# Kernel tuning notes

Measured on AMD Instinct MI355X. Metric: run time of the kernel, lower is better.

## Reference

```python
import jax, jax.numpy as jnp
import numpy as np

B, S, H, HKV, D = 1, 1024, 32, 8, 128
HID = H * D
GROUPS = H // HKV
ALPHA_K, ALPHA_V = 0.5, 0.5
GAMMA_MIN, GAMMA_MAX = 0.5, 2.0
ETA_MIN, ETA_MAX = 0.5, 2.0
BETA_BIAS, BIAS_CAP = 1.0, 5.0
BETA_POST = 0.5
ROPE_THETA = 10000.0


def setup_inputs() -> dict:
    key = jax.random.key(0)
    ks = jax.random.split(key, 9)
    hidden_states = jax.random.normal(ks[0], (B, S, HID), jnp.float32) * 0.02
    # additive causal mask (LLaMA-style, large negative above diagonal)
    causal = jnp.tril(jnp.ones((S, S), dtype=bool))
    attention_mask = jnp.where(causal, 0.0, -1e9).astype(jnp.float32)[None, None]
    position_ids = jnp.arange(S, dtype=jnp.int32)[None]
    sq = 1.0 / np.sqrt(HID)
    Wq = jax.random.normal(ks[1], (HID, HID), jnp.float32) * sq
    Wk = jax.random.normal(ks[2], (HKV * D, HID), jnp.float32) * sq
    Wv = jax.random.normal(ks[3], (HKV * D, HID), jnp.float32) * sq
    Wo = jax.random.normal(ks[4], (HID, HID), jnp.float32) * sq
    prior = jax.random.uniform(ks[5], (S,), jnp.float32)  # per-key-position prior, in [0,1)
    head_mask_l1 = (jax.random.uniform(ks[6], (H,)) > 0.5).astype(jnp.float32)
    head_mask_l2 = (jax.random.uniform(ks[7], (H,)) > 0.5).astype(jnp.float32)
    return {"hidden_states": hidden_states, "attention_mask": attention_mask,
            "position_ids": position_ids, "Wq": Wq, "Wk": Wk, "Wv": Wv, "Wo": Wo,
            "prior": prior, "head_mask_l1": head_mask_l1, "head_mask_l2": head_mask_l2}


def _rope(position_ids):
    inv_freq = 1.0 / (ROPE_THETA ** (jnp.arange(0, D, 2, dtype=jnp.float32) / D))
    freqs = position_ids.astype(jnp.float32)[..., None] * inv_freq  # [B,S,D/2]
    emb = jnp.concatenate([freqs, freqs], axis=-1)                  # [B,S,D]
    return jnp.cos(emb)[:, None], jnp.sin(emb)[:, None]             # [B,1,S,D]


def _rotate_half(x):
    x1, x2 = x[..., : D // 2], x[..., D // 2:]
    return jnp.concatenate([-x2, x1], axis=-1)


def reference(hidden_states, attention_mask, position_ids, Wq, Wk, Wv, Wo,
              prior, head_mask_l1, head_mask_l2):
    b, s, _ = hidden_states.shape
    # projections (Linear without bias: x @ W.T)
    q = (hidden_states @ Wq.T).reshape(b, s, H, D).transpose(0, 2, 1, 3)     # [B,H,S,D]
    k = (hidden_states @ Wk.T).reshape(b, s, HKV, D).transpose(0, 2, 1, 3)   # [B,Hkv,S,D]
    v = (hidden_states @ Wv.T).reshape(b, s, HKV, D).transpose(0, 2, 1, 3)
    cos, sin = _rope(position_ids)
    q = q * cos + _rotate_half(q) * sin
    k = k * cos + _rotate_half(k) * sin
    # repeat_kv: expand KV heads to match query heads (GQA)
    k = jnp.repeat(k, GROUPS, axis=1)  # [B,H,S,D]
    v = jnp.repeat(v, GROUPS, axis=1)
    # level4_scale: per-key-position multiplicative scaling of K and V
    gamma = jnp.clip(1.0 + ALPHA_K * prior, GAMMA_MIN, GAMMA_MAX)  # [S]
    eta = jnp.clip(1.0 + ALPHA_V * prior, ETA_MIN, ETA_MAX)
    k = k * gamma[None, None, :, None]
    v = v * eta[None, None, :, None]
    # attention logits
    attn = jnp.einsum('bhqd,bhkd->bhqk', q, k) / np.sqrt(D)
    # level1_bias: capped additive bias on logits, blended per-head
    bias = jnp.clip(BETA_BIAS * prior, -BIAS_CAP, BIAS_CAP)        # [S] over key dim
    steered = attn + bias[None, None, None, :]
    attn = attn + (steered - attn) * head_mask_l1[None, :, None, None]
    # causal mask
    attn = attn + attention_mask
    probs = jax.nn.softmax(attn.astype(jnp.float32), axis=-1)
    # level2_post: post-softmax rescale + renormalize, blended per-head
    sp = probs * (1.0 + BETA_POST * prior)[None, None, None, :]
    sp = sp / jnp.sum(sp, axis=-1, keepdims=True)
    probs = probs + (sp - probs) * head_mask_l2[None, :, None, None]
    out = jnp.einsum('bhqk,bhkd->bhqd', probs, v)                  # [B,H,S,D]
    out = out.transpose(0, 2, 1, 3).reshape(b, s, HID)
    return out @ Wo.T
```

## Files before the change

### kernel.cpp

```cpp
#include <hip/hip_runtime.h>
#include <math.h>

#define S_LEN 1024
#define HID_DIM 4096
#define NH 32
#define NKV 8
#define DH 128

typedef __attribute__((ext_vector_type(8))) short sh8;
typedef __attribute__((ext_vector_type(4))) short sh4;
typedef __attribute__((ext_vector_type(4))) float f4;

__device__ __forceinline__ unsigned short f2bf(float x) {
    union { float f; unsigned int u; } v; v.f = x;
    unsigned int r = v.u + 0x7FFFu + ((v.u >> 16) & 1u);
    return (unsigned short)(r >> 16);
}

__device__ __forceinline__ void gl_lds16(const unsigned short* g, unsigned short* l) {
    __builtin_amdgcn_global_load_lds(
        (const __attribute__((address_space(1))) unsigned int*)g,
        (__attribute__((address_space(3))) unsigned int*)l, 16, 0, 0);
}


__global__ void cvt_hw(const float* __restrict__ hidden, const float* __restrict__ Wq,
                       const float* __restrict__ Wk, const float* __restrict__ Wv,
                       unsigned short* __restrict__ hbf, unsigned short* __restrict__ wbuf)
{
    const int idx = blockIdx.x * 256 + threadIdx.x;
    const int NH4 = (S_LEN * HID_DIM) / 4;
    float4 v;
    sh4* dst;
    if (idx < NH4) {
        v = ((const float4*)hidden)[idx];
        dst = (sh4*)hbf + idx;
    } else {
        const int j = idx - NH4;
        const int row = j >> 10;
        if (row < 4096)      v = ((const float4*)Wq)[j];
        else if (row < 5120) v = ((const float4*)Wk)[j - 4096 * 1024];
        else                 v = ((const float4*)Wv)[j - 5120 * 1024];
        dst = (sh4*)wbuf + j;
    }
    sh4 o;
    o.x = (short)f2bf(v.x); o.y = (short)f2bf(v.y);
    o.z = (short)f2bf(v.z); o.w = (short)f2bf(v.w);
    *dst = o;
}

__global__ void cvt_wo(const float* __restrict__ Wo, unsigned short* __restrict__ wbuf)
{
    const int idx = blockIdx.x * 256 + threadIdx.x;
    const float4 v = ((const float4*)Wo)[idx];
    sh4 o;
    o.x = (short)f2bf(v.x); o.y = (short)f2bf(v.y);
    o.z = (short)f2bf(v.z); o.w = (short)f2bf(v.w);
    ((sh4*)wbuf)[idx] = o;
}

__global__ __launch_bounds__(256)
void gemm_bf16(const unsigned short* __restrict__ A, const unsigned short* __restrict__ B,
               float* __restrict__ C, int K, int kslices, int ldc)
{
    __shared__ __attribute__((aligned(16))) unsigned short sA[128 * 32];
    __shared__ __attribute__((aligned(16))) unsigned short sB[128 * 32];

    const int tid  = threadIdx.x;
    const int wave = tid >> 6;
    const int lane = tid & 63;
    const int l15  = lane & 15;
    const int quad = lane >> 4;
    const int m0   = blockIdx.y * 128;
    const int n0   = blockIdx.x * 128;
    const int wm   = (wave >> 1) * 64;
    const int wn   = (wave & 1) * 64;

    const int kchunk = K / kslices;
    const int kbeg = blockIdx.z * kchunk;
    const int kend = kbeg + kchunk;

    const int srow = wave * 32 + (lane >> 2);
    const int scol = (lane & 3) * 8;
    const unsigned short* Ag = A + (size_t)(m0 + srow) * K + scol;
    const unsigned short* Bg = B + (size_t)(n0 + srow) * K + scol;
    unsigned short* sAw = &sA[wave * 32 * 32];
    unsigned short* sBw = &sB[wave * 32 * 32];

    f4 acc[4][4];
#pragma unroll
    for (int i = 0; i < 4; i++)
#pragma unroll
        for (int j = 0; j < 4; j++)
            acc[i][j] = f4{0.0f, 0.0f, 0.0f, 0.0f};

    for (int k0 = kbeg; k0 < kend; k0 += 32) {
        __syncthreads();
        gl_lds16(Ag + k0,          sAw);
        gl_lds16(Ag + 16 * K + k0, sAw + 16 * 32);
        gl_lds16(Bg + k0,          sBw);
        gl_lds16(Bg + 16 * K + k0, sBw + 16 * 32);
        __syncthreads();

        sh8 af[4], bf[4];
#pragma unroll
        for (int i = 0; i < 4; i++)
            af[i] = *(const sh8*)(&sA[(wm + i * 16 + l15) * 32 + quad * 8]);
#pragma unroll
        for (int j = 0; j < 4; j++)
            bf[j] = *(const sh8*)(&sB[(wn + j * 16 + l15) * 32 + quad * 8]);
#pragma unroll
        for (int i = 0; i < 4; i++)
#pragma unroll
            for (int j = 0; j < 4; j++)
                acc[i][j] = __builtin_amdgcn_mfma_f32_16x16x32_bf16(af[i], bf[j], acc[i][j], 0, 0, 0);
    }

#pragma unroll
    for (int i = 0; i < 4; i++) {
        const int mrow = m0 + wm + i * 16 + quad * 4;
#pragma unroll
        for (int j = 0; j < 4; j++) {
            const int ncol = n0 + wn + j * 16 + l15;
            if (kslices == 1) {
#pragma unroll
                for (int r = 0; r < 4; r++)
                    C[(size_t)(mrow + r) * ldc + ncol] = acc[i][j][r];
            } else {
#pragma unroll
                for (int r = 0; r < 4; r++)
                    atomicAdd(&C[(size_t)(mrow + r) * ldc + ncol], acc[i][j][r]);
            }
        }
    }
}

__global__ void prep2(const float* __restrict__ qkv, const int* __restrict__ pos_ids,
                      const float* __restrict__ prior,
                      unsigned short* __restrict__ Qb, unsigned short* __restrict__ Kb,
                      unsigned short* __restrict__ Vt, float* __restrict__ addvT)
{
    const int idx = blockIdx.x * blockDim.x + threadIdx.x;
    const int NQ = S_LEN * 40 * 64;
    const int NV = S_LEN * NKV * DH;
    if (idx < NQ) {
        const int s   = idx / (40 * 64);
        const int rem = idx % (40 * 64);
        const int hh  = rem >> 6;
        const int i   = rem & 63;
        const float pos  = (float)pos_ids[s];
        const float invf = exp2f(-13.287712379549449f * (i * 0.015625f));
        const float ph = pos * invf;
        const float c = cosf(ph), sn = sinf(ph);
        if (hh < NH) {
            const float* base = qkv + (size_t)s * 6144 + hh * 128;
            const float x1 = base[i], x2 = base[i + 64];
            const float sc = 0.08838834764831845f * 1.4426950408889634f;
            unsigned short* q = Qb + ((size_t)hh * S_LEN + s) * DH;
            q[i]      = f2bf((x1 * c - x2 * sn) * sc);
            q[i + 64] = f2bf((x2 * c + x1 * sn) * sc);
        } else {
            const int kvh = hh - NH;
            const float* base = qkv + (size_t)s * 6144 + 4096 + kvh * 128;
            const float p = prior[s];
            const float gamma = fminf(fmaxf(1.0f + 0.5f * p, 0.5f), 2.0f);
            const float x1 = base[i], x2 = base[i + 64];
            unsigned short* kp = Kb + ((size_t)kvh * S_LEN + s) * DH;
            kp[i]      = f2bf((x1 * c - x2 * sn) * gamma);
            kp[i + 64] = f2bf((x2 * c + x1 * sn) * gamma);
        }
    } else if (idx < NQ + NV) {
        const int j = idx - NQ;
        const int s   = j / (NKV * DH);
        const int rem = j % (NKV * DH);
        const int kvh = rem >> 7;
        const int d   = rem & 127;
        const float p = prior[s];
        const float eta = fminf(fmaxf(1.0f + 0.5f * p, 0.5f), 2.0f);
        const float val = qkv[(size_t)s * 6144 + 5120 + kvh * 128 + d] * eta;
        Vt[((size_t)kvh * DH + d) * S_LEN + s] = f2bf(val);
    } else {
        const int j2 = idx - NQ - NV;
        if (j2 < 4 * S_LEN) {
            const int c = j2 >> 10;
            const int s = j2 & 1023;
            const float p = prior[s];
            const float bias = fminf(fmaxf(p, -5.0f), 5.0f);
            float v = 0.0f;
            if (c & 1) v += bias;
            if (c & 2) v += log1pf(0.5f * p);
            addvT[j2] = v * 1.4426950408889634f;
        }
    }
}

__global__ __launch_bounds__(256)
void attn4(const unsigned short* __restrict__ Qb, const unsigned short* __restrict__ Kb,
           const unsigned short* __restrict__ Vt, const float* __restrict__ addvT,
           const float* __restrict__ hm1, const float* __restrict__ hm2,
           unsigned short* __restrict__ ctx)
{
    __shared__ __attribute__((aligned(16))) unsigned short sK[32 * 128];
    __shared__ __attribute__((aligned(16))) unsigned short sV[128 * 32];
    __shared__ __attribute__((aligned(16))) short sP[4][16 * 40];

    const int h    = blockIdx.x;
    const int qb   = blockIdx.y;
    const int tid  = threadIdx.x;
    const int wave = tid >> 6;
    const int lane = tid & 63;
    const int l15  = lane & 15;
    const int quad = lane >> 4;
    const int q0   = qb * 64 + wave * 16;
    const int kvh  = h >> 2;
    const int combo = (hm1[h] > 0.5f ? 1 : 0) + (hm2[h] > 0.5f ? 2 : 0);
    const float* av = addvT + combo * S_LEN;

    const unsigned short* ksrc0 = Kb + ((size_t)kvh * S_LEN + (lane >> 4)) * DH + (lane & 15) * 8;
    const unsigned short* vsrc0 = Vt + ((size_t)kvh * DH + (lane >> 2)) * S_LEN + (lane & 3) * 8;

    sh8 qf[4];
    {
        const unsigned short* qbase = Qb + ((size_t)h * S_LEN + q0 + l15) * DH + quad * 8;
#pragma unroll
        for (int kc = 0; kc < 4; kc++)
            qf[kc] = *(const sh8*)(qbase + kc * 32);
    }

    f4 O[8];
#pragma unroll
    for (int dt = 0; dt < 8; dt++) O[dt] = f4{0.0f, 0.0f, 0.0f, 0.0f};
    float lrun[4] = {0.0f, 0.0f, 0.0f, 0.0f};

    short* pl = &sP[wave][0];
    const int nch = 2 * qb + 2;

    for (int c = 0; c < nch; c++) {
        const int k0 = c * 32;
        __syncthreads();
        if (wave < 2) {
            const unsigned short* ks = ksrc0 + (size_t)k0 * DH;
#pragma unroll
            for (int j = 0; j < 4; j++) {
                const int i = wave * 4 + j;
                gl_lds16(ks + (size_t)(4 * i) * DH, &sK[i * 512]);
            }
        } else {
            const unsigned short* vs = vsrc0 + k0;
#pragma unroll
            for (int j = 0; j < 4; j++) {
                const int i = (wave - 2) * 4 + j;
                gl_lds16(vs + (size_t)(16 * i) * S_LEN, &sV[i * 512]);
            }
        }
        __syncthreads();

        float e[2][4];
#pragma unroll
        for (int t = 0; t < 2; t++) {
            f4 a = f4{0.0f, 0.0f, 0.0f, 0.0f};
#pragma unroll
            for (int kc = 0; kc < 4; kc++) {
                const sh8 kfr = *(const sh8*)(&sK[(t * 16 + l15) * 128 + kc * 32 + quad * 8]);
                a = __builtin_amdgcn_mfma_f32_16x16x32_bf16(qf[kc], kfr, a, 0, 0, 0);
            }
            const int key = k0 + t * 16 + l15;
            const float ad = av[key];
#pragma unroll
            for (int r = 0; r < 4; r++) {
                const int qrow = q0 + quad * 4 + r;
                float ex = exp2f(a[r] + ad);
                ex = (key <= qrow) ? ex : 0.0f;
                e[t][r] = ex;
                lrun[r] += ex;
                pl[(quad * 4 + r) * 40 + t * 16 + l15] = (short)f2bf(ex);
            }
        }
        asm volatile("s_waitcnt lgkmcnt(0)" ::: "memory");
        const sh8 ap = *(const sh8*)(&pl[l15 * 40 + quad * 8]);
#pragma unroll
        for (int dt = 0; dt < 8; dt++) {
            const sh8 vfr = *(const sh8*)(&sV[(dt * 16 + l15) * 32 + quad * 8]);
            O[dt] = __builtin_amdgcn_mfma_f32_16x16x32_bf16(ap, vfr, O[dt], 0, 0, 0);
        }
    }

#pragma unroll
    for (int r = 0; r < 4; r++) {
        float l = lrun[r];
        l += __shfl_xor(l, 1); l += __shfl_xor(l, 2);
        l += __shfl_xor(l, 4); l += __shfl_xor(l, 8);
        const float inv = 1.0f / l;
        const int row = q0 + quad * 4 + r;
        unsigned short* cp = ctx + (size_t)row * HID_DIM + h * DH;
#pragma unroll
        for (int dt = 0; dt < 8; dt++)
            cp[dt * 16 + l15] = f2bf(O[dt][r] * inv);
    }
}


#define LDSW 40

__global__ __launch_bounds__(256)
void gemm_bt(const float* __restrict__ A,
             const float* __restrict__ B0, const float* __restrict__ B1,
             const float* __restrict__ B2, int n_b1, int n_b2,
             float* __restrict__ C, int M, int N, int K, int ldc)
{
    __shared__ __attribute__((aligned(16))) short sA[128 * LDSW];
    __shared__ __attribute__((aligned(16))) short sB[128 * LDSW];
    const int tid  = threadIdx.x;
    const int m0   = blockIdx.y * 128;
    const int n0   = blockIdx.x * 128;
    const float* Bp = B0; int nloc = n0;
    if (n0 >= n_b2)      { Bp = B2; nloc = n0 - n_b2; }
    else if (n0 >= n_b1) { Bp = B1; nloc = n0 - n_b1; }
    const int wave = tid >> 6, lane = tid & 63;
    const int l15 = lane & 15, quad = lane >> 4;
    const int wm = (wave >> 1) * 64, wn = (wave & 1) * 64;
    const int rb = tid >> 3, c4 = (tid & 7) * 4;
    f4 acc[4][4];
#pragma unroll
    for (int i = 0; i < 4; i++)
#pragma unroll
        for (int j = 0; j < 4; j++) acc[i][j] = f4{0.0f, 0.0f, 0.0f, 0.0f};
    for (int k0 = 0; k0 < K; k0 += 32) {
        __syncthreads();
#pragma unroll
        for (int i = 0; i < 4; i++) {
            const int row = rb + 32 * i;
            const float4 va = *(const float4*)(A  + (size_t)(m0 + row) * K + k0 + c4);
            const float4 vb = *(const float4*)(Bp + (size_t)(nloc + row) * K + k0 + c4);
            sh4 sa, sb;
            sa.x = (short)f2bf(va.x); sa.y = (short)f2bf(va.y);
            sa.z = (short)f2bf(va.z); sa.w = (short)f2bf(va.w);
            sb.x = (short)f2bf(vb.x); sb.y = (short)f2bf(vb.y);
            sb.z = (short)f2bf(vb.z); sb.w = (short)f2bf(vb.w);
            *(sh4*)(&sA[row * LDSW + c4]) = sa;
            *(sh4*)(&sB[row * LDSW + c4]) = sb;
        }
        __syncthreads();
        sh8 af[4], bf[4];
#pragma unroll
        for (int i = 0; i < 4; i++) af[i] = *(const sh8*)(&sA[(wm + i * 16 + l15) * LDSW + quad * 8]);
#pragma unroll
        for (int j = 0; j < 4; j++) bf[j] = *(const sh8*)(&sB[(wn + j * 16 + l15) * LDSW + quad * 8]);
#pragma unroll
        for (int i = 0; i < 4; i++)
#pragma unroll
            for (int j = 0; j < 4; j++)
                acc[i][j] = __builtin_amdgcn_mfma_f32_16x16x32_bf16(af[i], bf[j], acc[i][j], 0, 0, 0);
    }
#pragma unroll
    for (int i = 0; i < 4; i++) {
        const int mrow = m0 + wm + i * 16 + quad * 4;
#pragma unroll
        for (int j = 0; j < 4; j++) {
            const int ncol = n0 + wn + j * 16 + l15;
#pragma unroll
            for (int r = 0; r < 4; r++)
                C[(size_t)(mrow + r) * ldc + ncol] = acc[i][j][r];
        }
    }
}

__global__ void prep_rope(const float* __restrict__ qkv, const int* __restrict__ pos_ids,
                          const float* __restrict__ prior,
                          unsigned short* __restrict__ Qb, unsigned short* __restrict__ Kb,
                          unsigned short* __restrict__ Vt)
{
    const int idx = blockIdx.x * blockDim.x + threadIdx.x;
    const int NQ = S_LEN * 40 * 64;
    if (idx < NQ) {
        const int s = idx / (40 * 64);
        const int rem = idx % (40 * 64);
        const int hh = rem >> 6, i = rem & 63;
        const float pos = (float)pos_ids[s];
        const float invf = exp2f(-13.287712379549449f * (i * 0.015625f));
        const float ph = pos * invf;
        const float c = cosf(ph), sn = sinf(ph);
        if (hh < NH) {
            const float* base = qkv + (size_t)s * 6144 + hh * 128;
            const float x1 = base[i], x2 = base[i + 64];
            const float sc = 0.08838834764831845f;
            unsigned short* q = Qb + ((size_t)hh * S_LEN + s) * DH;
            q[i] = f2bf((x1 * c - x2 * sn) * sc);
            q[i + 64] = f2bf((x2 * c + x1 * sn) * sc);
        } else {
            const int kvh = hh - NH;
            const float* base = qkv + (size_t)s * 6144 + 4096 + kvh * 128;
            const float p = prior[s];
            const float gamma = fminf(fmaxf(1.0f + 0.5f * p, 0.5f), 2.0f);
            const float x1 = base[i], x2 = base[i + 64];
            unsigned short* kp = Kb + ((size_t)kvh * S_LEN + s) * DH;
            kp[i] = f2bf((x1 * c - x2 * sn) * gamma);
            kp[i + 64] = f2bf((x2 * c + x1 * sn) * gamma);
        }
    } else {
        const int j = idx - NQ;
        if (j < S_LEN * NKV * DH) {
            const int s = j / (NKV * DH);
            const int rem = j % (NKV * DH);
            const int kvh = rem >> 7, d = rem & 127;
            const float p = prior[s];
            const float eta = fminf(fmaxf(1.0f + 0.5f * p, 0.5f), 2.0f);
            const float val = qkv[(size_t)s * 6144 + 5120 + kvh * 128 + d] * eta;
            Vt[((size_t)kvh * DH + d) * S_LEN + s] = f2bf(val);
        }
    }
}

__global__ __launch_bounds__(256)
void attn_kernel(const unsigned short* __restrict__ Qb, const unsigned short* __restrict__ Kb,
                 const unsigned short* __restrict__ Vt, const float* __restrict__ prior,
                 const float* __restrict__ hm1, const float* __restrict__ hm2,
                 float* __restrict__ ctx)
{
    __shared__ __attribute__((aligned(16))) short p_lds[4][16 * LDSW];
    const int h = blockIdx.x, qb = blockIdx.y;
    const int wave = threadIdx.x >> 6, lane = threadIdx.x & 63;
    const int l15 = lane & 15, quad = lane >> 4;
    const int q0 = qb * 64 + wave * 16;
    const int kvh = h >> 2;
    const float m1 = hm1[h], m2 = hm2[h];
    const float NEG = -3.0e38f;
    sh8 qf[4];
    {
        const unsigned short* qbase = Qb + ((size_t)h * S_LEN + q0 + l15) * DH + quad * 8;
#pragma unroll
        for (int kc = 0; kc < 4; kc++) qf[kc] = *(const sh8*)(qbase + kc * 32);
    }
    f4 O[8];
#pragma unroll
    for (int dt = 0; dt < 8; dt++) O[dt] = f4{0.0f, 0.0f, 0.0f, 0.0f};
    float mrun[4], lrun[4];
#pragma unroll
    for (int r = 0; r < 4; r++) { mrun[r] = NEG; lrun[r] = 0.0f; }
    short* pl = &p_lds[wave][0];
    const int qmax = q0 + 15;
    for (int key0 = 0; key0 <= qmax; key0 += 32) {
        float sc[2][4];
#pragma unroll
        for (int t = 0; t < 2; t++) {
            const int kt = key0 + t * 16;
            const unsigned short* kb = Kb + ((size_t)kvh * S_LEN + kt + l15) * DH + quad * 8;
            f4 a = f4{0.0f, 0.0f, 0.0f, 0.0f};
#pragma unroll
            for (int kc = 0; kc < 4; kc++) {
                const sh8 bfr = *(const sh8*)(kb + kc * 32);
                a = __builtin_amdgcn_mfma_f32_16x16x32_bf16(qf[kc], bfr, a, 0, 0, 0);
            }
            const int key = kt + l15;
            const float p = prior[key];
            const float bias = fminf(fmaxf(p, -5.0f), 5.0f);
            const float addv = m1 * bias + m2 * logf(1.0f + 0.5f * p);
#pragma unroll
            for (int r = 0; r < 4; r++) {
                const int qrow = q0 + quad * 4 + r;
                sc[t][r] = (key <= qrow) ? (a[r] + addv) : NEG;
            }
        }
        float cm[4], mnew[4], alpha[4], rs[4];
#pragma unroll
        for (int r = 0; r < 4; r++) {
            cm[r] = fmaxf(sc[0][r], sc[1][r]);
            cm[r] = fmaxf(cm[r], __shfl_xor(cm[r], 1));
            cm[r] = fmaxf(cm[r], __shfl_xor(cm[r], 2));
            cm[r] = fmaxf(cm[r], __shfl_xor(cm[r], 4));
            cm[r] = fmaxf(cm[r], __shfl_xor(cm[r], 8));
            mnew[r] = fmaxf(mrun[r], cm[r]);
            alpha[r] = expf(mrun[r] - mnew[r]);
        }
        float e[2][4];
#pragma unroll
        for (int t = 0; t < 2; t++)
#pragma unroll
            for (int r = 0; r < 4; r++) e[t][r] = expf(sc[t][r] - mnew[r]);
#pragma unroll
        for (int r = 0; r < 4; r++) {
            rs[r] = e[0][r] + e[1][r];
            rs[r] += __shfl_xor(rs[r], 1); rs[r] += __shfl_xor(rs[r], 2);
            rs[r] += __shfl_xor(rs[r], 4); rs[r] += __shfl_xor(rs[r], 8);
            lrun[r] = lrun[r] * alpha[r] + rs[r];
            mrun[r] = mnew[r];
        }
#pragma unroll
        for (int dt = 0; dt < 8; dt++)
#pragma unroll
            for (int r = 0; r < 4; r++) O[dt][r] *= alpha[r];
#pragma unroll
        for (int t = 0; t < 2; t++)
#pragma unroll
            for (int r = 0; r < 4; r++)
                pl[(quad * 4 + r) * LDSW + t * 16 + l15] = (short)f2bf(e[t][r]);
        asm volatile("s_waitcnt lgkmcnt(0)" ::: "memory");
        const sh8 ap = *(const sh8*)(&pl[l15 * LDSW + quad * 8]);
        const unsigned short* vb = Vt + ((size_t)kvh * DH + l15) * S_LEN + key0 + quad * 8;
#pragma unroll
        for (int dt = 0; dt < 8; dt++) {
            const sh8 bfv = *(const sh8*)(vb + (size_t)dt * 16 * S_LEN);
            O[dt] = __builtin_amdgcn_mfma_f32_16x16x32_bf16(ap, bfv, O[dt], 0, 0, 0);
        }
    }
#pragma unroll
    for (int r = 0; r < 4; r++) {
        const float inv = 1.0f / lrun[r];
        const int row = q0 + quad * 4 + r;
        float* cp = ctx + (size_t)row * HID_DIM + h * DH;
#pragma unroll
        for (int dt = 0; dt < 8; dt++) cp[dt * 16 + l15] = O[dt][r] * inv;
    }
}


extern "C" void kernel_launch(void* const* d_in, const int* in_sizes, int n_in,
                              void* d_out, int out_size, void* d_ws, size_t ws_size,
                              hipStream_t stream)
{
    const float* hidden  = (const float*)d_in[0];
    const int*   pos_ids = (const int*)d_in[2];
    const float* Wq = (const float*)d_in[3];
    const float* Wk = (const float*)d_in[4];
    const float* Wv = (const float*)d_in[5];
    const float* Wo = (const float*)d_in[6];
    const float* prior = (const float*)d_in[7];
    const float* hm1 = (const float*)d_in[8];
    const float* hm2 = (const float*)d_in[9];
    float* out = (float*)d_out;
    char* ws = (char*)d_ws;

    const size_t FAST_NEED = 96485376ull;
    if (ws_size >= FAST_NEED) {
        unsigned short* Wbuf = (unsigned short*)ws;
        unsigned short* Cbf  = (unsigned short*)(ws + 33554432);
        unsigned short* Hbf  = (unsigned short*)(ws + 50331648);
        float*          qkv  = (float*)(ws + 58720256);
        unsigned short* Qb   = (unsigned short*)(ws + 83886080);
        unsigned short* Kb   = (unsigned short*)(ws + 92274688);
        unsigned short* Vt   = (unsigned short*)(ws + 94371840);
        float*          addv = (float*)(ws + 96468992);

        hipMemsetAsync(qkv, 0, 25165824, stream);
        hipMemsetAsync(out, 0, 16777216, stream);
        cvt_hw<<<28672, 256, 0, stream>>>(hidden, Wq, Wk, Wv, Hbf, Wbuf);
        gemm_bf16<<<dim3(48, 8, 2), 256, 0, stream>>>(Hbf, Wbuf, qkv, 4096, 2, 6144);
        prep2<<<14352, 256, 0, stream>>>(qkv, pos_ids, prior, Qb, Kb, Vt, addv);
        cvt_wo<<<16384, 256, 0, stream>>>(Wo, Wbuf);
        attn4<<<dim3(32, 16), 256, 0, stream>>>(Qb, Kb, Vt, addv, hm1, hm2, Cbf);
        gemm_bf16<<<dim3(32, 8, 4), 256, 0, stream>>>(Cbf, Wbuf, out, 4096, 4, 4096);
    } else {
        float*          qkv = (float*)ws;
        float*          ctx = (float*)(ws + 25165824);
        unsigned short* Qb  = (unsigned short*)(ws + 41943040);
        unsigned short* Kb  = (unsigned short*)(ws + 50331648);
        unsigned short* Vt  = (unsigned short*)(ws + 52428800);
        gemm_bt<<<dim3(48, 8), 256, 0, stream>>>(hidden, Wq, Wk, Wv, 4096, 5120,
                                                 qkv, 1024, 6144, 4096, 6144);
        prep_rope<<<14336, 256, 0, stream>>>(qkv, pos_ids, prior, Qb, Kb, Vt);
        attn_kernel<<<dim3(32, 16), 256, 0, stream>>>(Qb, Kb, Vt, prior, hm1, hm2, ctx);
        gemm_bt<<<dim3(32, 8), 256, 0, stream>>>(ctx, Wo, Wo, Wo, 1 << 30, 1 << 30,
                                                 out, 1024, 4096, 4096, 4096);
    }
}
```

Before: 449.0 us.

## XOR-swizzle LDS tiles and widen GEMM k-step to 64

The bf16 GEMM now loads a 64-wide k slice per iteration into shared memory, with an XOR-swizzled column layout. This halves the number of barrier pairs and is meant to avoid LDS bank conflicts on the MFMA fragment reads. The attention kernel applies matching XOR swizzles to the K and V tiles, so the global-to-LDS loads write permuted chunks and the fragment reads undo the permutation. LDS use per GEMM block doubles, which could lower occupancy.

```diff
diff --git a/kernel.cpp b/kernel.cpp
--- a/kernel.cpp
+++ b/kernel.cpp
@@ -60,11 +60,11 @@
 }
 
 __global__ __launch_bounds__(256)
-void gemm_bf16(const unsigned short* __restrict__ A, const unsigned short* __restrict__ B,
-               float* __restrict__ C, int K, int kslices, int ldc)
-{
-    __shared__ __attribute__((aligned(16))) unsigned short sA[128 * 32];
-    __shared__ __attribute__((aligned(16))) unsigned short sB[128 * 32];
+void gemm64(const unsigned short* __restrict__ A, const unsigned short* __restrict__ B,
+            float* __restrict__ C, int K, int kslices, int ldc)
+{
+    __shared__ __attribute__((aligned(16))) unsigned short sA[128 * 64];
+    __shared__ __attribute__((aligned(16))) unsigned short sB[128 * 64];
 
     const int tid  = threadIdx.x;
     const int wave = tid >> 6;
@@ -80,12 +80,12 @@
     const int kbeg = blockIdx.z * kchunk;
     const int kend = kbeg + kchunk;
 
-    const int srow = wave * 32 + (lane >> 2);
-    const int scol = (lane & 3) * 8;
-    const unsigned short* Ag = A + (size_t)(m0 + srow) * K + scol;
-    const unsigned short* Bg = B + (size_t)(n0 + srow) * K + scol;
-    unsigned short* sAw = &sA[wave * 32 * 32];
-    unsigned short* sBw = &sB[wave * 32 * 32];
+    const int rloc = lane >> 3;
+    const int clog = (lane & 7) ^ rloc;
+    const unsigned short* Ag = A + (size_t)(m0 + wave * 32 + rloc) * K + clog * 8;
+    const unsigned short* Bg = B + (size_t)(n0 + wave * 32 + rloc) * K + clog * 8;
+    unsigned short* sAw = &sA[wave * 32 * 64];
+    unsigned short* sBw = &sB[wave * 32 * 64];
 
     f4 acc[4][4];
 #pragma unroll
@@ -94,26 +94,32 @@
         for (int j = 0; j < 4; j++)
             acc[i][j] = f4{0.0f, 0.0f, 0.0f, 0.0f};
 
-    for (int k0 = kbeg; k0 < kend; k0 += 32) {
+    const int sw = l15 & 7;
+
+    for (int k0 = kbeg; k0 < kend; k0 += 64) {
         __syncthreads();
-        gl_lds16(Ag + k0,          sAw);
-        gl_lds16(Ag + 16 * K + k0, sAw + 16 * 32);
-        gl_lds16(Bg + k0,          sBw);
-        gl_lds16(Bg + 16 * K + k0, sBw + 16 * 32);
+#pragma unroll
+        for (int j = 0; j < 4; j++) {
+            gl_lds16(Ag + k0 + (size_t)(j * 8) * K, sAw + j * 8 * 64);
+            gl_lds16(Bg + k0 + (size_t)(j * 8) * K, sBw + j * 8 * 64);
+        }
         __syncthreads();
 
-        sh8 af[4], bf[4];
-#pragma unroll
-        for (int i = 0; i < 4; i++)
-            af[i] = *(const sh8*)(&sA[(wm + i * 16 + l15) * 32 + quad * 8]);
-#pragma unroll
-        for (int j = 0; j < 4; j++)
-            bf[j] = *(const sh8*)(&sB[(wn + j * 16 + l15) * 32 + quad * 8]);
-#pragma unroll
-        for (int i = 0; i < 4; i++)
+#pragma unroll
+        for (int ks = 0; ks < 2; ks++) {
+            sh8 af[4], bf[4];
+#pragma unroll
+            for (int i = 0; i < 4; i++)
+                af[i] = *(const sh8*)(&sA[(wm + i * 16 + l15) * 64 + ((ks * 4 + quad) ^ sw) * 8]);
 #pragma unroll
             for (int j = 0; j < 4; j++)
-                acc[i][j] = __builtin_amdgcn_mfma_f32_16x16x32_bf16(af[i], bf[j], acc[i][j], 0, 0, 0);
+                bf[j] = *(const sh8*)(&sB[(wn + j * 16 + l15) * 64 + ((ks * 4 + quad) ^ sw) * 8]);
+#pragma unroll
+            for (int i = 0; i < 4; i++)
+#pragma unroll
+                for (int j = 0; j < 4; j++)
+                    acc[i][j] = __builtin_amdgcn_mfma_f32_16x16x32_bf16(af[i], bf[j], acc[i][j], 0, 0, 0);
+        }
     }
 
 #pragma unroll
@@ -195,7 +201,7 @@
 }
 
 __global__ __launch_bounds__(256)
-void attn4(const unsigned short* __restrict__ Qb, const unsigned short* __restrict__ Kb,
+void attn5(const unsigned short* __restrict__ Qb, const unsigned short* __restrict__ Kb,
            const unsigned short* __restrict__ Vt, const float* __restrict__ addvT,
            const float* __restrict__ hm1, const float* __restrict__ hm2,
            unsigned short* __restrict__ ctx)
@@ -216,8 +222,12 @@
     const int combo = (hm1[h] > 0.5f ? 1 : 0) + (hm2[h] > 0.5f ? 2 : 0);
     const float* av = addvT + combo * S_LEN;
 
-    const unsigned short* ksrc0 = Kb + ((size_t)kvh * S_LEN + (lane >> 4)) * DH + (lane & 15) * 8;
-    const unsigned short* vsrc0 = Vt + ((size_t)kvh * DH + (lane >> 2)) * S_LEN + (lane & 3) * 8;
+    const unsigned short* ksrcE = Kb + ((size_t)kvh * S_LEN + (lane >> 4)) * DH
+                                  + (((lane & 15) ^ (lane >> 4)) * 8);
+    const unsigned short* ksrcO = Kb + ((size_t)kvh * S_LEN + (lane >> 4)) * DH
+                                  + (((lane & 15) ^ (4 + (lane >> 4))) * 8);
+    const unsigned short* vsrc0 = Vt + ((size_t)kvh * DH + (lane >> 2)) * S_LEN
+                                  + (((lane & 3) ^ ((lane >> 2) & 3)) * 8);
 
     sh8 qf[4];
     {
@@ -233,35 +243,35 @@
     float lrun[4] = {0.0f, 0.0f, 0.0f, 0.0f};
 
     short* pl = &sP[wave][0];
+    const int sw = l15 & 7;
+    const int sv = l15 & 3;
     const int nch = 2 * qb + 2;
 
     for (int c = 0; c < nch; c++) {
         const int k0 = c * 32;
         __syncthreads();
         if (wave < 2) {
-            const unsigned short* ks = ksrc0 + (size_t)k0 * DH;
 #pragma unroll
             for (int j = 0; j < 4; j++) {
                 const int i = wave * 4 + j;
-                gl_lds16(ks + (size_t)(4 * i) * DH, &sK[i * 512]);
+                const unsigned short* src = (j & 1) ? ksrcO : ksrcE;
+                gl_lds16(src + (size_t)(k0 + 4 * i) * DH, &sK[i * 512]);
             }
         } else {
-            const unsigned short* vs = vsrc0 + k0;
 #pragma unroll
             for (int j = 0; j < 4; j++) {
                 const int i = (wave - 2) * 4 + j;
-                gl_lds16(vs + (size_t)(16 * i) * S_LEN, &sV[i * 512]);
+                gl_lds16(vsrc0 + (size_t)(16 * i) * S_LEN + k0, &sV[i * 512]);
             }
         }
         __syncthreads();
 
-        float e[2][4];
 #pragma unroll
         for (int t = 0; t < 2; t++) {
             f4 a = f4{0.0f, 0.0f, 0.0f, 0.0f};
 #pragma unroll
             for (int kc = 0; kc < 4; kc++) {
-                const sh8 kfr = *(const sh8*)(&sK[(t * 16 + l15) * 128 + kc * 32 + quad * 8]);
+                const sh8 kfr = *(const sh8*)(&sK[(t * 16 + l15) * 128 + ((kc * 4 + quad) ^ sw) * 8]);
                 a = __builtin_amdgcn_mfma_f32_16x16x32_bf16(qf[kc], kfr, a, 0, 0, 0);
             }
             const int key = k0 + t * 16 + l15;
@@ -271,7 +281,6 @@
                 const int qrow = q0 + quad * 4 + r;
                 float ex = exp2f(a[r] + ad);
                 ex = (key <= qrow) ? ex : 0.0f;
-                e[t][r] = ex;
                 lrun[r] += ex;
                 pl[(quad * 4 + r) * 40 + t * 16 + l15] = (short)f2bf(ex);
             }
@@ -280,7 +289,7 @@
         const sh8 ap = *(const sh8*)(&pl[l15 * 40 + quad * 8]);
 #pragma unroll
         for (int dt = 0; dt < 8; dt++) {
-            const sh8 vfr = *(const sh8*)(&sV[(dt * 16 + l15) * 32 + quad * 8]);
+            const sh8 vfr = *(const sh8*)(&sV[(dt * 16 + l15) * 32 + (quad ^ sv) * 8]);
             O[dt] = __builtin_amdgcn_mfma_f32_16x16x32_bf16(ap, vfr, O[dt], 0, 0, 0);
         }
     }
@@ -544,11 +553,11 @@
         hipMemsetAsync(qkv, 0, 25165824, stream);
         hipMemsetAsync(out, 0, 16777216, stream);
         cvt_hw<<<28672, 256, 0, stream>>>(hidden, Wq, Wk, Wv, Hbf, Wbuf);
-        gemm_bf16<<<dim3(48, 8, 2), 256, 0, stream>>>(Hbf, Wbuf, qkv, 4096, 2, 6144);
+        gemm64<<<dim3(48, 8, 2), 256, 0, stream>>>(Hbf, Wbuf, qkv, 4096, 2, 6144);
         prep2<<<14352, 256, 0, stream>>>(qkv, pos_ids, prior, Qb, Kb, Vt, addv);
         cvt_wo<<<16384, 256, 0, stream>>>(Wo, Wbuf);
-        attn4<<<dim3(32, 16), 256, 0, stream>>>(Qb, Kb, Vt, addv, hm1, hm2, Cbf);
-        gemm_bf16<<<dim3(32, 8, 4), 256, 0, stream>>>(Cbf, Wbuf, out, 4096, 4, 4096);
+        attn5<<<dim3(32, 16), 256, 0, stream>>>(Qb, Kb, Vt, addv, hm1, hm2, Cbf);
+        gemm64<<<dim3(32, 8, 4), 256, 0, stream>>>(Cbf, Wbuf, out, 4096, 4, 4096);
     } else {
         float*          qkv = (float*)ws;
         float*          ctx = (float*)(ws + 25165824);
```

Result: no change. 454.6 us (+1.2%).
